# Kernel tuning notes

Hardware: AMD Instinct MI355X
Metric: run time of the kernel (lower is better)

The kernel has to match this reference:

```python
import jax, jax.numpy as jnp
import numpy as np

NUM_VOCAB = 50000
EMBED_DIM = 128
SENT_SIZE = 50
MAX_HOPS = 3
BATCH = 128
MEM_SIZE = 200


def position_encoding(sentence_size, embedding_dim):
    # vectorized version of the original double loop
    i = np.arange(1, embedding_dim + 1, dtype=np.float32)[:, None]  # [D,1]
    j = np.arange(1, sentence_size + 1, dtype=np.float32)[None, :]  # [1,S]
    enc = (i - (embedding_dim + 1) / 2.0) * (j - (sentence_size + 1) / 2.0)
    enc = 1.0 + 4.0 * enc / embedding_dim / sentence_size
    enc[:, -1] = 1.0
    return np.transpose(enc).astype(np.float32)  # [S,D]


def setup_inputs() -> dict:
    key = jax.random.key(0)
    k1, k2, k3, k4, k5 = jax.random.split(key, 5)
    story = jax.random.randint(k1, (BATCH, MEM_SIZE, SENT_SIZE), 0, NUM_VOCAB, dtype=jnp.int64)
    query = jax.random.randint(k2, (BATCH, SENT_SIZE), 0, NUM_VOCAB, dtype=jnp.int64)
    # max_hops+1 embedding tables, N(0, 0.1), padding_idx=0 row zeroed
    C = 0.1 * jax.random.normal(k3, (MAX_HOPS + 1, NUM_VOCAB, EMBED_DIM), dtype=jnp.float32)
    C = C.at[:, 0, :].set(0.0)
    # T_k linear layer (PyTorch default uniform init bound)
    bound = 1.0 / np.sqrt(EMBED_DIM)
    T_w = jax.random.uniform(k4, (EMBED_DIM, EMBED_DIM), jnp.float32, -bound, bound)
    T_b = jax.random.uniform(k5, (EMBED_DIM,), jnp.float32, -bound, bound)
    return {"story": story, "query": query, "C": C, "T_w": T_w, "T_b": T_b}


def reference(story, query, C, T_w, T_b):
    enc = jnp.asarray(position_encoding(SENT_SIZE, EMBED_DIM))  # [S,D]
    # u0: position-encoded sum of query embedding
    q_emb = C[0][query]  # [B,S,D]
    u = jnp.einsum('bsd,sd->bd', q_emb, enc)
    for hop in range(MAX_HOPS):
        emb_A = C[hop][story]          # [B,M,S,D]
        m_A = jnp.einsum('bmsd,sd->bmd', emb_A, enc)
        prob = jax.nn.softmax(jnp.einsum('bmd,bd->bm', m_A, u), axis=-1)
        emb_C = C[hop + 1][story]      # [B,M,S,D]
        m_C = jnp.einsum('bmsd,sd->bmd', emb_C, enc)
        o_k = jnp.einsum('bmd,bm->bd', m_C, prob)
        t_k = jax.nn.sigmoid(u @ T_w.T + T_b)
        u = (1.0 - t_k) * u + o_k * t_k
    a_hat = u @ C[MAX_HOPS].T  # [B,V]
    return a_hat
```

## Files before the change

kernel.cpp:

```cpp
#include <hip/hip_runtime.h>
#include <cstdint>
#include <cstddef>

#define NV 50000
#define ED 128
#define SS 50
#define NB 128
#define NM 200
#define BMD (NB*NM*ED)
#define NCH 32
#define CHD 1563

typedef _Float16 f16x8 __attribute__((ext_vector_type(8)));
typedef _Float16 f16x4 __attribute__((ext_vector_type(4)));
typedef _Float16 f16x2 __attribute__((ext_vector_type(2)));
typedef float    f32x4 __attribute__((ext_vector_type(4)));

__global__ __launch_bounds__(256) void cvt_c3_k(
    const float* __restrict__ src, _Float16* __restrict__ dst) {
  const int i = blockIdx.x * 256 + threadIdx.x;
  const float4* s4 = (const float4*)src;
  float4 f0 = s4[2 * (size_t)i];
  float4 f1 = s4[2 * (size_t)i + 1];
  f16x8 h;
  h[0] = (_Float16)f0.x; h[1] = (_Float16)f0.y;
  h[2] = (_Float16)f0.z; h[3] = (_Float16)f0.w;
  h[4] = (_Float16)f1.x; h[5] = (_Float16)f1.y;
  h[6] = (_Float16)f1.z; h[7] = (_Float16)f1.w;
  *(f16x8*)(dst + (size_t)8 * i) = h;
}

__global__ __launch_bounds__(256) void story_embed_k(
    const int* __restrict__ story, const float* __restrict__ C,
    const _Float16* __restrict__ C3h, float* __restrict__ Mt) {
  const int wave = threadIdx.x >> 6;
  const int lane = threadIdx.x & 63;
  const int bm0 = blockIdx.x * 8;
  const int sl = (lane < SS) ? lane : (SS - 1);

  int idxg[2], cidg[2];
#pragma unroll
  for (int gg = 0; gg < 2; ++gg) {
    const int bm = bm0 + wave + 4 * gg;
    idxg[gg] = story[(size_t)bm * SS + sl];
    cidg[gg] = (lane < SS) ? (idxg[gg] / CHD) : -1;
  }
  const float a0 = ((float)(2*lane + 1) - 64.5f) * 6.25e-4f;
  const float a1 = ((float)(2*lane + 2) - 64.5f) * 6.25e-4f;
  float2 acc[2][4];
#pragma unroll
  for (int gg = 0; gg < 2; ++gg)
#pragma unroll
    for (int k = 0; k < 4; ++k) acc[gg][k] = make_float2(0.f, 0.f);

  for (int c = 0; c < NCH; ++c) {
#pragma unroll
    for (int gg = 0; gg < 2; ++gg) {
      unsigned long long mask = __ballot(cidg[gg] == c);
      while (mask) {
        const int s = __builtin_ctzll(mask);
        mask &= mask - 1;
        const int row = __shfl(idxg[gg], s);
        float e0, e1;
        if (s == SS - 1) { e0 = 1.0f; e1 = 1.0f; }
        else {
          float js = (float)(s + 1) - 25.5f;
          e0 = fmaf(a0, js, 1.0f);
          e1 = fmaf(a1, js, 1.0f);
        }
        const float* base = C + (size_t)row * ED + 2 * lane;
#pragma unroll
        for (int k = 0; k < 3; ++k) {
          float2 cv = *(const float2*)(base + (size_t)k * NV * ED);
          acc[gg][k].x = fmaf(e0, cv.x, acc[gg][k].x);
          acc[gg][k].y = fmaf(e1, cv.y, acc[gg][k].y);
        }
        f16x2 cv3 = *(const f16x2*)(C3h + (size_t)row * ED + 2 * lane);
        acc[gg][3].x = fmaf(e0, (float)cv3[0], acc[gg][3].x);
        acc[gg][3].y = fmaf(e1, (float)cv3[1], acc[gg][3].y);
      }
    }
    __syncthreads();
  }

#pragma unroll
  for (int gg = 0; gg < 2; ++gg) {
    const int bm = bm0 + wave + 4 * gg;
#pragma unroll
    for (int k = 0; k < 4; ++k)
      *(float2*)(Mt + (size_t)k * BMD + (size_t)bm * ED + 2 * lane) = acc[gg][k];
  }
}

__global__ __launch_bounds__(512, 2) void hops_k(
    const int* __restrict__ query, const float* __restrict__ C,
    const float* __restrict__ Tw, const float* __restrict__ Tb,
    const float* __restrict__ Mt, float* __restrict__ U) {
  const int b = blockIdx.x;
  const int tid = threadIdx.x;
  const int d = tid & 127;
  const int p = tid >> 7;
  const int wave = tid >> 6, lane = tid & 63;
  __shared__ float tile[NM * ED];
  __shared__ float u[ED];
  __shared__ float part[512];
  __shared__ float sc[NM];
  __shared__ float o[ED];

  {
    const float4* s4 = (const float4*)(Mt + (size_t)b * NM * ED);
    float4* t4 = (float4*)tile;
    float4 st[13];
#pragma unroll
    for (int j = 0; j < 13; ++j) {
      int i = tid + 512 * j;
      st[j] = (i < NM * ED / 4) ? s4[i] : make_float4(0.f, 0.f, 0.f, 0.f);
    }
#pragma unroll
    for (int j = 0; j < 13; ++j) {
      int i = tid + 512 * j;
      if (i < NM * ED / 4) t4[i] = st[j];
    }
  }

  {
    const float ad = ((float)(d + 1) - 64.5f) * 6.25e-4f;
    int rows[13];
#pragma unroll
    for (int j = 0; j < 13; ++j) {
      int s = p + 4 * j;
      rows[j] = query[b * SS + (s < SS ? s : 0)];
    }
    float cv[13];
#pragma unroll
    for (int j = 0; j < 13; ++j)
      cv[j] = C[(size_t)rows[j] * ED + d];
    float accv = 0.f;
#pragma unroll
    for (int j = 0; j < 13; ++j) {
      int s = p + 4 * j;
      float e;
      if (s >= SS) e = 0.f;
      else if (s == SS - 1) e = 1.0f;
      else e = fmaf(ad, (float)(s + 1) - 25.5f, 1.0f);
      accv = fmaf(e, cv[j], accv);
    }
    part[tid] = accv;
  }
  __syncthreads();
  if (tid < ED)
    u[tid] = part[tid] + part[tid + 128] + part[tid + 256] + part[tid + 384];
  __syncthreads();

  for (int hop = 0; hop < 3; ++hop) {
    const float* Tn = Mt + (size_t)(hop + 1) * BMD + (size_t)b * NM * ED;
    float pf[50];
#pragma unroll
    for (int j = 0; j < 50; ++j)
      pf[j] = Tn[(size_t)(p + 4 * j) * ED + d];

    {
      float u0v = u[2 * lane], u1v = u[2 * lane + 1];
      for (int m = wave; m < NM; m += 16) {
        const int m2 = m + 8;
        const bool has2 = (m2 < NM);
        float2 r0 = *(const float2*)&tile[m * ED + 2 * lane];
        float pa = r0.x * u0v + r0.y * u1v;
        float pb = 0.f;
        if (has2) {
          float2 r1 = *(const float2*)&tile[m2 * ED + 2 * lane];
          pb = r1.x * u0v + r1.y * u1v;
        }
#pragma unroll
        for (int off = 32; off; off >>= 1) {
          pa += __shfl_xor(pa, off);
          pb += __shfl_xor(pb, off);
        }
        if (lane == 0) {
          sc[m] = pa;
          if (has2) sc[m2] = pb;
        }
      }
    }
    __syncthreads();

    float v = (tid < NM) ? sc[tid] : -1e30f;
    {
      float t = v;
#pragma unroll
      for (int off = 32; off; off >>= 1) t = fmaxf(t, __shfl_xor(t, off));
      if (lane == 0) part[wave] = t;
    }
    __syncthreads();
    float mx = part[0];
#pragma unroll
    for (int w = 1; w < 8; ++w) mx = fmaxf(mx, part[w]);
    float ev = 0.f;
    if (tid < NM) { ev = __expf(v - mx); sc[tid] = ev; }
    {
      float t = ev;
#pragma unroll
      for (int off = 32; off; off >>= 1) t += __shfl_xor(t, off);
      if (lane == 0) part[8 + wave] = t;
    }
    __syncthreads();
    float tot = part[8];
#pragma unroll
    for (int w = 9; w < 16; ++w) tot += part[w];
    const float inv = 1.0f / tot;
    __syncthreads();

    {
      float oacc = 0.f;
#pragma unroll
      for (int j = 0; j < 50; ++j)
        oacc = fmaf(sc[p + 4 * j], pf[j], oacc);
      part[tid] = oacc;
    }
    if (hop < 2) {
#pragma unroll
      for (int j = 0; j < 50; ++j)
        tile[(p + 4 * j) * ED + d] = pf[j];
    }
    __syncthreads();
    if (tid < ED)
      o[tid] = (part[tid] + part[tid + 128] + part[tid + 256] + part[tid + 384])
               * inv;
    __syncthreads();

    {
      const float4* twr = (const float4*)(Tw + (size_t)d * ED + p * 32);
      float4 tw4[8];
#pragma unroll
      for (int j = 0; j < 8; ++j) tw4[j] = twr[j];
      float tacc = 0.f;
#pragma unroll
      for (int j = 0; j < 8; ++j) {
        tacc = fmaf(u[p * 32 + 4 * j + 0], tw4[j].x, tacc);
        tacc = fmaf(u[p * 32 + 4 * j + 1], tw4[j].y, tacc);
        tacc = fmaf(u[p * 32 + 4 * j + 2], tw4[j].z, tacc);
        tacc = fmaf(u[p * 32 + 4 * j + 3], tw4[j].w, tacc);
      }
      part[tid] = tacc;
    }
    __syncthreads();
    if (tid < ED) {
      float dot = part[tid] + part[tid + 128] + part[tid + 256] + part[tid + 384]
                  + Tb[tid];
      float tk = 1.0f / (1.0f + __expf(-dot));
      u[tid] = (1.0f - tk) * u[tid] + o[tid] * tk;
    }
    __syncthreads();
  }
  if (tid < ED) U[(size_t)b * ED + tid] = u[tid];
}

__global__ __launch_bounds__(512) void out_mm_mfma_k(
    const float* __restrict__ U, const _Float16* __restrict__ C3h,
    float* __restrict__ out) {
  __shared__ _Float16 Ub[ED * 136];
  const int tid = threadIdx.x;

  {
    const float4* u4 = (const float4*)U;
#pragma unroll
    for (int j = 0; j < 8; ++j) {
      int i = tid + 512 * j;
      float4 f = u4[i];
      int row = i >> 5;
      int col = (i & 31) * 4;
      f16x4 h;
      h[0] = (_Float16)f.x; h[1] = (_Float16)f.y;
      h[2] = (_Float16)f.z; h[3] = (_Float16)f.w;
      *(f16x4*)&Ub[row * 136 + col] = h;
    }
  }
  __syncthreads();

  const int wave = tid >> 6, lane = tid & 63;
  const int n = lane & 15, q = lane >> 4;
  const int v = blockIdx.x * 128 + wave * 16 + n;
  const bool vok = (v < NV);

  f32x4 acc[8];
#pragma unroll
  for (int mt = 0; mt < 8; ++mt) acc[mt] = (f32x4){0.f, 0.f, 0.f, 0.f};

#pragma unroll
  for (int kt = 0; kt < 4; ++kt) {
    f16x8 bfrag = {};
    if (vok) bfrag = *(const f16x8*)(C3h + (size_t)v * ED + kt * 32 + q * 8);
#pragma unroll
    for (int mt = 0; mt < 8; ++mt) {
      f16x8 afrag = *(const f16x8*)&Ub[(mt * 16 + n) * 136 + kt * 32 + q * 8];
      acc[mt] = __builtin_amdgcn_mfma_f32_16x16x32_f16(afrag, bfrag, acc[mt],
                                                       0, 0, 0);
    }
  }

  if (vok) {
#pragma unroll
    for (int mt = 0; mt < 8; ++mt)
#pragma unroll
      for (int i = 0; i < 4; ++i)
        out[(size_t)(mt * 16 + q * 4 + i) * NV + v] = acc[mt][i];
  }
}

extern "C" void kernel_launch(void* const* d_in, const int* in_sizes, int n_in,
                              void* d_out, int out_size, void* d_ws, size_t ws_size,
                              hipStream_t stream) {
  const int*   story = (const int*)d_in[0];
  const int*   query = (const int*)d_in[1];
  const float* C     = (const float*)d_in[2];
  const float* Tw    = (const float*)d_in[3];
  const float* Tb    = (const float*)d_in[4];
  float* out = (float*)d_out;

  float* wsf = (float*)d_ws;
  float*     Mt  = wsf;
  float*     U   = wsf + (size_t)4 * BMD;
  _Float16*  C3h = (_Float16*)(wsf + (size_t)4 * BMD + NB * ED);

  hipLaunchKernelGGL(cvt_c3_k, dim3(NV * ED / 8 / 256), dim3(256), 0, stream,
                     C + (size_t)3 * NV * ED, C3h);
  hipLaunchKernelGGL(story_embed_k, dim3(NB * NM / 8), dim3(256), 0, stream,
                     story, C, C3h, Mt);
  hipLaunchKernelGGL(hops_k, dim3(NB), dim3(512), 0, stream,
                     query, C, Tw, Tb, Mt, U);
  hipLaunchKernelGGL(out_mm_mfma_k, dim3((NV + 127) / 128), dim3(512), 0, stream,
                     U, C3h, out);
}
```

Before: 394.3 us.

## Split story embedding per table across blocks and prefetch all hop tiles upfront

The story embedding kernel now gives each block a single table and 16 memory slots instead of all four tables for 8 slots. This doubles the grid and lowers per-lane accumulator pressure, so more blocks run in parallel and each one touches a smaller working set. The hops kernel loads all three next-hop tiles into registers before the hop loop and unrolls the hops with a macro, so the global loads overlap with the query embedding and softmax work. This costs about 150 extra live registers per thread and risks spilling under launch_bounds(512,2). The story indices and the chunk ballot loop are also repeated once per table.

After: 588.1 us. +49.2%, slower.

```diff
diff --git a/kernel.cpp b/kernel.cpp
--- a/kernel.cpp
+++ b/kernel.cpp
@@ -33,29 +33,34 @@
 __global__ __launch_bounds__(256) void story_embed_k(
     const int* __restrict__ story, const float* __restrict__ C,
     const _Float16* __restrict__ C3h, float* __restrict__ Mt) {
+  const int s8    = blockIdx.x & 7;
+  const int table = s8 >> 1;
+  const int bmset = (blockIdx.x >> 3) * 2 + (s8 & 1);
   const int wave = threadIdx.x >> 6;
   const int lane = threadIdx.x & 63;
-  const int bm0 = blockIdx.x * 8;
+  const int bm0 = bmset * 16;
   const int sl = (lane < SS) ? lane : (SS - 1);
 
-  int idxg[2], cidg[2];
-#pragma unroll
-  for (int gg = 0; gg < 2; ++gg) {
+  int idxg[4], cidg[4];
+#pragma unroll
+  for (int gg = 0; gg < 4; ++gg) {
     const int bm = bm0 + wave + 4 * gg;
     idxg[gg] = story[(size_t)bm * SS + sl];
     cidg[gg] = (lane < SS) ? (idxg[gg] / CHD) : -1;
   }
   const float a0 = ((float)(2*lane + 1) - 64.5f) * 6.25e-4f;
   const float a1 = ((float)(2*lane + 2) - 64.5f) * 6.25e-4f;
-  float2 acc[2][4];
-#pragma unroll
-  for (int gg = 0; gg < 2; ++gg)
-#pragma unroll
-    for (int k = 0; k < 4; ++k) acc[gg][k] = make_float2(0.f, 0.f);
+  float2 acc[4];
+#pragma unroll
+  for (int gg = 0; gg < 4; ++gg) acc[gg] = make_float2(0.f, 0.f);
+
+  const float* Ct = C + (size_t)table * NV * ED + 2 * lane;
+  const _Float16* C3t = C3h + 2 * lane;
+  const bool t3 = (table == 3);
 
   for (int c = 0; c < NCH; ++c) {
 #pragma unroll
-    for (int gg = 0; gg < 2; ++gg) {
+    for (int gg = 0; gg < 4; ++gg) {
       unsigned long long mask = __ballot(cidg[gg] == c);
       while (mask) {
         const int s = __builtin_ctzll(mask);
@@ -68,27 +73,25 @@
           e0 = fmaf(a0, js, 1.0f);
           e1 = fmaf(a1, js, 1.0f);
         }
-        const float* base = C + (size_t)row * ED + 2 * lane;
-#pragma unroll
-        for (int k = 0; k < 3; ++k) {
-          float2 cv = *(const float2*)(base + (size_t)k * NV * ED);
-          acc[gg][k].x = fmaf(e0, cv.x, acc[gg][k].x);
-          acc[gg][k].y = fmaf(e1, cv.y, acc[gg][k].y);
+        float cx, cy;
+        if (t3) {
+          f16x2 cv = *(const f16x2*)(C3t + (size_t)row * ED);
+          cx = (float)cv[0]; cy = (float)cv[1];
+        } else {
+          float2 cv = *(const float2*)(Ct + (size_t)row * ED);
+          cx = cv.x; cy = cv.y;
         }
-        f16x2 cv3 = *(const f16x2*)(C3h + (size_t)row * ED + 2 * lane);
-        acc[gg][3].x = fmaf(e0, (float)cv3[0], acc[gg][3].x);
-        acc[gg][3].y = fmaf(e1, (float)cv3[1], acc[gg][3].y);
+        acc[gg].x = fmaf(e0, cx, acc[gg].x);
+        acc[gg].y = fmaf(e1, cy, acc[gg].y);
       }
     }
     __syncthreads();
   }
 
 #pragma unroll
-  for (int gg = 0; gg < 2; ++gg) {
+  for (int gg = 0; gg < 4; ++gg) {
     const int bm = bm0 + wave + 4 * gg;
-#pragma unroll
-    for (int k = 0; k < 4; ++k)
-      *(float2*)(Mt + (size_t)k * BMD + (size_t)bm * ED + 2 * lane) = acc[gg][k];
+    *(float2*)(Mt + (size_t)table * BMD + (size_t)bm * ED + 2 * lane) = acc[gg];
   }
 }
 
@@ -123,6 +126,19 @@
     }
   }
 
+  float pf0[50], pf1[50], pf2[50];
+  {
+    const float* T1 = Mt + (size_t)1 * BMD + (size_t)b * NM * ED;
+    const float* T2 = Mt + (size_t)2 * BMD + (size_t)b * NM * ED;
+    const float* T3 = Mt + (size_t)3 * BMD + (size_t)b * NM * ED;
+#pragma unroll
+    for (int j = 0; j < 50; ++j) pf0[j] = T1[(size_t)(p + 4 * j) * ED + d];
+#pragma unroll
+    for (int j = 0; j < 50; ++j) pf1[j] = T2[(size_t)(p + 4 * j) * ED + d];
+#pragma unroll
+    for (int j = 0; j < 50; ++j) pf2[j] = T3[(size_t)(p + 4 * j) * ED + d];
+  }
+
   {
     const float ad = ((float)(d + 1) - 64.5f) * 6.25e-4f;
     int rows[13];
@@ -152,106 +168,104 @@
     u[tid] = part[tid] + part[tid + 128] + part[tid + 256] + part[tid + 384];
   __syncthreads();
 
-  for (int hop = 0; hop < 3; ++hop) {
-    const float* Tn = Mt + (size_t)(hop + 1) * BMD + (size_t)b * NM * ED;
-    float pf[50];
-#pragma unroll
-    for (int j = 0; j < 50; ++j)
-      pf[j] = Tn[(size_t)(p + 4 * j) * ED + d];
-
-    {
-      float u0v = u[2 * lane], u1v = u[2 * lane + 1];
-      for (int m = wave; m < NM; m += 16) {
-        const int m2 = m + 8;
-        const bool has2 = (m2 < NM);
-        float2 r0 = *(const float2*)&tile[m * ED + 2 * lane];
-        float pa = r0.x * u0v + r0.y * u1v;
-        float pb = 0.f;
-        if (has2) {
-          float2 r1 = *(const float2*)&tile[m2 * ED + 2 * lane];
-          pb = r1.x * u0v + r1.y * u1v;
-        }
-#pragma unroll
-        for (int off = 32; off; off >>= 1) {
-          pa += __shfl_xor(pa, off);
-          pb += __shfl_xor(pb, off);
-        }
-        if (lane == 0) {
-          sc[m] = pa;
-          if (has2) sc[m2] = pb;
-        }
-      }
-    }
-    __syncthreads();
-
-    float v = (tid < NM) ? sc[tid] : -1e30f;
-    {
-      float t = v;
-#pragma unroll
-      for (int off = 32; off; off >>= 1) t = fmaxf(t, __shfl_xor(t, off));
-      if (lane == 0) part[wave] = t;
-    }
-    __syncthreads();
-    float mx = part[0];
-#pragma unroll
-    for (int w = 1; w < 8; ++w) mx = fmaxf(mx, part[w]);
-    float ev = 0.f;
-    if (tid < NM) { ev = __expf(v - mx); sc[tid] = ev; }
-    {
-      float t = ev;
-#pragma unroll
-      for (int off = 32; off; off >>= 1) t += __shfl_xor(t, off);
-      if (lane == 0) part[8 + wave] = t;
-    }
-    __syncthreads();
-    float tot = part[8];
-#pragma unroll
-    for (int w = 9; w < 16; ++w) tot += part[w];
-    const float inv = 1.0f / tot;
-    __syncthreads();
-
-    {
-      float oacc = 0.f;
-#pragma unroll
-      for (int j = 0; j < 50; ++j)
-        oacc = fmaf(sc[p + 4 * j], pf[j], oacc);
-      part[tid] = oacc;
-    }
-    if (hop < 2) {
-#pragma unroll
-      for (int j = 0; j < 50; ++j)
-        tile[(p + 4 * j) * ED + d] = pf[j];
-    }
-    __syncthreads();
-    if (tid < ED)
-      o[tid] = (part[tid] + part[tid + 128] + part[tid + 256] + part[tid + 384])
-               * inv;
-    __syncthreads();
-
-    {
-      const float4* twr = (const float4*)(Tw + (size_t)d * ED + p * 32);
-      float4 tw4[8];
-#pragma unroll
-      for (int j = 0; j < 8; ++j) tw4[j] = twr[j];
-      float tacc = 0.f;
-#pragma unroll
-      for (int j = 0; j < 8; ++j) {
-        tacc = fmaf(u[p * 32 + 4 * j + 0], tw4[j].x, tacc);
-        tacc = fmaf(u[p * 32 + 4 * j + 1], tw4[j].y, tacc);
-        tacc = fmaf(u[p * 32 + 4 * j + 2], tw4[j].z, tacc);
-        tacc = fmaf(u[p * 32 + 4 * j + 3], tw4[j].w, tacc);
-      }
-      part[tid] = tacc;
-    }
-    __syncthreads();
-    if (tid < ED) {
-      float dot = part[tid] + part[tid + 128] + part[tid + 256] + part[tid + 384]
-                  + Tb[tid];
-      float tk = 1.0f / (1.0f + __expf(-dot));
-      u[tid] = (1.0f - tk) * u[tid] + o[tid] * tk;
-    }
-    __syncthreads();
-  }
+#define HOP_BODY(PF, UPDATE_TILE)                                             \
+  {                                                                           \
+    {                                                                         \
+      float u0v = u[2 * lane], u1v = u[2 * lane + 1];                         \
+      for (int m = wave; m < NM; m += 16) {                                   \
+        const int m2 = m + 8;                                                 \
+        const bool has2 = (m2 < NM);                                          \
+        float2 r0 = *(const float2*)&tile[m * ED + 2 * lane];                 \
+        float pa = r0.x * u0v + r0.y * u1v;                                   \
+        float pb = 0.f;                                                       \
+        if (has2) {                                                           \
+          float2 r1 = *(const float2*)&tile[m2 * ED + 2 * lane];              \
+          pb = r1.x * u0v + r1.y * u1v;                                       \
+        }                                                                     \
+        _Pragma("unroll")                                                     \
+        for (int off = 32; off; off >>= 1) {                                  \
+          pa += __shfl_xor(pa, off);                                          \
+          pb += __shfl_xor(pb, off);                                          \
+        }                                                                     \
+        if (lane == 0) {                                                      \
+          sc[m] = pa;                                                         \
+          if (has2) sc[m2] = pb;                                              \
+        }                                                                     \
+      }                                                                       \
+    }                                                                         \
+    __syncthreads();                                                          \
+    float v = (tid < NM) ? sc[tid] : -1e30f;                                  \
+    {                                                                         \
+      float t = v;                                                            \
+      _Pragma("unroll")                                                       \
+      for (int off = 32; off; off >>= 1) t = fmaxf(t, __shfl_xor(t, off));    \
+      if (lane == 0) part[wave] = t;                                          \
+    }                                                                         \
+    __syncthreads();                                                          \
+    float mx = part[0];                                                       \
+    _Pragma("unroll")                                                         \
+    for (int w = 1; w < 8; ++w) mx = fmaxf(mx, part[w]);                      \
+    float ev = 0.f;                                                           \
+    if (tid < NM) { ev = __expf(v - mx); sc[tid] = ev; }                      \
+    {                                                                         \
+      float t = ev;                                                           \
+      _Pragma("unroll")                                                       \
+      for (int off = 32; off; off >>= 1) t += __shfl_xor(t, off);             \
+      if (lane == 0) part[8 + wave] = t;                                      \
+    }                                                                         \
+    __syncthreads();                                                          \
+    float tot = part[8];                                                      \
+    _Pragma("unroll")                                                         \
+    for (int w = 9; w < 16; ++w) tot += part[w];                              \
+    const float inv = 1.0f / tot;                                             \
+    __syncthreads();                                                          \
+    {                                                                         \
+      float oacc = 0.f;                                                       \
+      _Pragma("unroll")                                                       \
+      for (int j = 0; j < 50; ++j)                                            \
+        oacc = fmaf(sc[p + 4 * j], PF[j], oacc);                              \
+      part[tid] = oacc;                                                       \
+    }                                                                         \
+    if (UPDATE_TILE) {                                                        \
+      _Pragma("unroll")                                                       \
+      for (int j = 0; j < 50; ++j)                                            \
+        tile[(p + 4 * j) * ED + d] = PF[j];                                   \
+    }                                                                         \
+    __syncthreads();                                                          \
+    if (tid < ED)                                                             \
+      o[tid] = (part[tid] + part[tid + 128] + part[tid + 256]                 \
+                + part[tid + 384]) * inv;                                     \
+    __syncthreads();                                                          \
+    {                                                                         \
+      const float4* twr = (const float4*)(Tw + (size_t)d * ED + p * 32);      \
+      float4 tw4[8];                                                          \
+      _Pragma("unroll")                                                       \
+      for (int j = 0; j < 8; ++j) tw4[j] = twr[j];                            \
+      float tacc = 0.f;                                                       \
+      _Pragma("unroll")                                                       \
+      for (int j = 0; j < 8; ++j) {                                           \
+        tacc = fmaf(u[p * 32 + 4 * j + 0], tw4[j].x, tacc);                   \
+        tacc = fmaf(u[p * 32 + 4 * j + 1], tw4[j].y, tacc);                   \
+        tacc = fmaf(u[p * 32 + 4 * j + 2], tw4[j].z, tacc);                   \
+        tacc = fmaf(u[p * 32 + 4 * j + 3], tw4[j].w, tacc);                   \
+      }                                                                       \
+      part[tid] = tacc;                                                       \
+    }                                                                         \
+    __syncthreads();                                                          \
+    if (tid < ED) {                                                           \
+      float dot = part[tid] + part[tid + 128] + part[tid + 256]               \
+                  + part[tid + 384] + Tb[tid];                                \
+      float tk = 1.0f / (1.0f + __expf(-dot));                                \
+      u[tid] = (1.0f - tk) * u[tid] + o[tid] * tk;                            \
+    }                                                                         \
+    __syncthreads();                                                          \
+  }
+
+  HOP_BODY(pf0, true)
+  HOP_BODY(pf1, true)
+  HOP_BODY(pf2, false)
+#undef HOP_BODY
+
   if (tid < ED) U[(size_t)b * ED + tid] = u[tid];
 }
 
@@ -324,8 +338,8 @@
 
   hipLaunchKernelGGL(cvt_c3_k, dim3(NV * ED / 8 / 256), dim3(256), 0, stream,
                      C + (size_t)3 * NV * ED, C3h);
-  hipLaunchKernelGGL(story_embed_k, dim3(NB * NM / 8), dim3(256), 0, stream,
-                     story, C, C3h, Mt);
+  hipLaunchKernelGGL(story_embed_k, dim3(4 * NB * NM / 16), dim3(256), 0,
+                     stream, story, C, C3h, Mt);
   hipLaunchKernelGGL(hops_k, dim3(NB), dim3(512), 0, stream,
                      query, C, Tw, Tb, Mt, U);
   hipLaunchKernelGGL(out_mm_mfma_k, dim3((NV + 127) / 128), dim3(512), 0, stream,
```
